# Optimization experiments

Hardware: AMD Instinct MI355X
Metric: run time of the kernel (lower is better)

Reference implementation:

```python
import jax, jax.numpy as jnp
import numpy as np

N = 128          # system size (8*8*2), hard-coded in SpectrumLoss
M_LANCZOS = 10   # Lanczos(m=10)
KAPPA = 0.276


def dd_opt(x, U1, kappa):
    # Wilson-style 2D hopping operator (stand-in for the external DDOpt).
    # x: (B,8,8,2) fields, U1: (B,8,8,2) real gauge links (2 directions).
    u0 = U1[..., 0:1]
    u1 = U1[..., 1:2]
    hop = (u0 * jnp.roll(x, -1, axis=1)
           + u1 * jnp.roll(x, -1, axis=2)
           + jnp.roll(u0 * x, 1, axis=1)
           + jnp.roll(u1 * x, 1, axis=2))
    return x - kappa * hop


def build_lower_tri(net_out):
    # Row-major packing of a lower-triangular NxN matrix (torch.tril_indices order).
    B = net_out.shape[0]
    r, c = jnp.tril_indices(N)
    L = jnp.zeros((B, N, N), net_out.dtype)
    return L.at[:, r, c].set(net_out)


def matvect(L, U1, x):
    # x: (B, N). Preconditioned operator: L (L^T (D x)).
    B = x.shape[0]
    y = dd_opt(x.reshape(B, 8, 8, 2), U1, KAPPA).reshape(B, N)
    y = jnp.einsum('bij,bi->bj', L, y)  # upper_tri_mat: M^H v (real -> M^T v)
    y = jnp.einsum('bij,bj->bi', L, y)  # lower_tri_matvect: L v
    return y


def lanczos(Av, v0):
    # Standard batched Lanczos producing symmetric tridiagonal T (B, M, M).
    B = v0.shape[0]

    def step(carry, _):
        v_prev, v_cur, beta = carry
        w = Av(v_cur)
        alpha = jnp.sum(w * v_cur, axis=1)
        w = w - alpha[:, None] * v_cur - beta[:, None] * v_prev
        beta_new = jnp.linalg.norm(w, axis=1)
        v_next = w / (beta_new[:, None] + 1e-30)
        return (v_cur, v_next, beta_new), (alpha, beta_new)

    init = (jnp.zeros_like(v0), v0, jnp.zeros((B,), v0.dtype))
    _, (alphas, betas) = jax.lax.scan(step, init, None, length=M_LANCZOS)
    alphas = alphas.T  # (B, M)
    betas = betas.T    # (B, M); last beta unused
    T = jnp.zeros((B, M_LANCZOS, M_LANCZOS), v0.dtype)
    i = jnp.arange(M_LANCZOS)
    T = T.at[:, i, i].set(alphas)
    j = jnp.arange(M_LANCZOS - 1)
    T = T.at[:, j, j + 1].set(betas[:, :-1])
    T = T.at[:, j + 1, j].set(betas[:, :-1])
    return T


def setup_inputs() -> dict:
    key = jax.random.key(0)
    k1, k2, k3 = jax.random.split(key, 3)
    B = 2048
    net_out = jax.random.normal(k1, (B, N * (N + 1) // 2), dtype=jnp.float32)
    U1 = jax.random.uniform(k2, (B, 8, 8, 2), dtype=jnp.float32)
    v = jax.random.normal(k3, (B, N), dtype=jnp.float32)
    return {"net_out": net_out, "U1": U1, "v": v}


def reference(net_out, U1, v):
    vn = v / jnp.linalg.norm(v, axis=1, keepdims=True)
    L = build_lower_tri(net_out)
    T = lanczos(lambda x: matvect(L, U1, x), vn)
    eig = jnp.abs(jnp.linalg.eigvalsh(T))  # symmetric tridiagonal -> real eigvals
    max_e = jnp.max(eig, axis=1)
    min_e = jnp.min(eig, axis=1)
    return jnp.mean(max_e ** 2) - jnp.mean(min_e ** 2)
```

## Files before the change

kernel.cpp:

```cpp
#include <hip/hip_runtime.h>
#include <hip/hip_bf16.h>
#include <math.h>

#define NN 128
#define TRI 8256
#define BATCH 2048
#define M_L 10
#define KAPPA 0.276f
#define LDL 136

using half8  = __attribute__((ext_vector_type(8))) _Float16;
using half2v = __attribute__((ext_vector_type(2))) _Float16;
using f32x4  = __attribute__((ext_vector_type(4))) float;

static __device__ inline float dot2h(unsigned m, unsigned y, float c) {
#if __has_builtin(__builtin_amdgcn_fdot2)
    return __builtin_amdgcn_fdot2(__builtin_bit_cast(half2v, m),
                                  __builtin_bit_cast(half2v, y), c, false);
#else
    half2v a = __builtin_bit_cast(half2v, m), b = __builtin_bit_cast(half2v, y);
    return c + (float)a.x * (float)b.x + (float)a.y * (float)b.y;
#endif
}

__device__ inline int sturm_count10(const double* a, const double* off2, double x) {
    double pm = 1.0;
    double p  = a[0] - x;
    int c = (p < 0.0);
    #pragma unroll
    for (int i = 1; i < M_L; i++) {
        double pn = (a[i] - x) * p - off2[i - 1] * pm;
        c += ((pn < 0.0) != (p < 0.0));
        pm = p; p = pn;
    }
    return c;
}

__global__ __launch_bounds__(256, 4) void lanczos_kernel(
    const float* __restrict__ net_out,
    const float* __restrict__ U1,
    const float* __restrict__ v_in,
    float* __restrict__ contrib)
{
    __shared__ __align__(16) _Float16 Lsq[128 * LDL];
    __shared__ __align__(16) unsigned ys[64];
    __shared__ __align__(16) float part[256];
    __shared__ __align__(16) float ab_s[20];

    const int b = blockIdx.x;
    const int t = threadIdx.x;
    const int lane = t & 63;
    const int w = t >> 6;

    float2 vv = {0.f, 0.f}, uu = {0.f, 0.f};
    if (w == 0) {
        vv = *(const float2*)(v_in + (size_t)b * NN + 2 * lane);
        uu = *(const float2*)(U1 + (size_t)b * 128 + 2 * lane);
    }

    {
        unsigned long long* z = (unsigned long long*)Lsq;
        #pragma unroll
        for (int k = t; k < 128 * LDL / 4; k += 256) z[k] = 0ULL;
    }
    __syncthreads();

    {
        const float4* src4 = (const float4*)(net_out + (size_t)b * TRI);
        for (int q = t; q < TRI / 4; q += 256) {
            float4 f = src4[q];
            const int e = 4 * q;
            float vals[4] = {f.x, f.y, f.z, f.w};
            #pragma unroll
            for (int i = 0; i < 4; i++) {
                int ei = e + i;
                int r = (int)((sqrtf((float)(8 * ei) + 1.0f) - 1.0f) * 0.5f);
                int c = ei - ((r * (r + 1)) >> 1);
                Lsq[r * LDL + c] = (_Float16)vals[i];
            }
        }
    }
    __syncthreads();

    {
        const int m = lane & 15;
        const int g = lane >> 4;
        f32x4 acc[2][8];
        #pragma unroll
        for (int bi = 0; bi < 2; bi++)
            #pragma unroll
            for (int j = 0; j < 8; j++) acc[bi][j] = (f32x4){0.f, 0.f, 0.f, 0.f};
        const int band0 = w, band1 = w + 4;
        #pragma unroll
        for (int kc = 0; kc < 4; kc++) {
            const int col = kc * 32 + g * 8;
            half8 a0 = *(const half8*)&Lsq[(16 * band0 + m) * LDL + col];
            half8 a1 = *(const half8*)&Lsq[(16 * band1 + m) * LDL + col];
            #pragma unroll
            for (int j = 0; j < 8; j++) {
                half8 bfr = *(const half8*)&Lsq[(16 * j + m) * LDL + col];
                acc[0][j] = __builtin_amdgcn_mfma_f32_16x16x32_f16(a0, bfr, acc[0][j], 0, 0, 0);
                acc[1][j] = __builtin_amdgcn_mfma_f32_16x16x32_f16(a1, bfr, acc[1][j], 0, 0, 0);
            }
        }
        __syncthreads();

        #pragma unroll
        for (int bi = 0; bi < 2; bi++) {
            const int band = (bi == 0) ? band0 : band1;
            #pragma unroll
            for (int j = 0; j < 8; j++) {
                f32x4 a = acc[bi][j];
                half2v p01 = {(_Float16)a[0], (_Float16)a[1]};
                half2v p23 = {(_Float16)a[2], (_Float16)a[3]};
                uint2 pk;
                pk.x = __builtin_bit_cast(unsigned, p01);
                pk.y = __builtin_bit_cast(unsigned, p23);
                *(uint2*)&Lsq[(16 * j + m) * LDL + 16 * band + 4 * g] = pk;
            }
        }
    }
    __syncthreads();

    const int r = t & 127, h = t >> 7;
    uint4 Mr[8];
    {
        const uint4* M4 = (const uint4*)&Lsq[r * LDL + 64 * h];
        #pragma unroll
        for (int c = 0; c < 8; c++) Mr[c] = M4[c];
    }

    float x0 = 0.f, x1 = 0.f, p0 = 0.f, p1 = 0.f, beta = 0.f;
    float u0c = 0.f, u1c = 0.f, u0m = 0.f, u1m = 0.f;
    const int l_ip = (lane + 8) & 63;
    const int l_jp = (lane & 56) | ((lane + 1) & 7);
    const int l_im = (lane + 56) & 63;
    const int l_jm = (lane & 56) | ((lane + 7) & 7);

    if (w == 0) {
        float s = vv.x * vv.x + vv.y * vv.y;
        #pragma unroll
        for (int o = 1; o < 64; o <<= 1) s += __shfl_xor(s, o, 64);
        float inv = 1.0f / sqrtf(s);
        x0 = vv.x * inv; x1 = vv.y * inv;
        u0c = uu.x; u1c = uu.y;
        u0m = __shfl(u0c, l_im, 64);
        u1m = __shfl(u1c, l_jm, 64);

        float a0 = __shfl(x0, l_ip, 64), a1 = __shfl(x1, l_ip, 64);
        float b0 = __shfl(x0, l_jp, 64), b1 = __shfl(x1, l_jp, 64);
        float c0 = __shfl(x0, l_im, 64), c1 = __shfl(x1, l_im, 64);
        float d0 = __shfl(x0, l_jm, 64), d1 = __shfl(x1, l_jm, 64);
        float y0 = x0 - KAPPA * (u0c * a0 + u1c * b0 + u0m * c0 + u1m * d0);
        float y1 = x1 - KAPPA * (u0c * a1 + u1c * b1 + u0m * c1 + u1m * d1);
        half2v yp = {(_Float16)y0, (_Float16)y1};
        ys[lane] = __builtin_bit_cast(unsigned, yp);
    }
    __syncthreads();

    const uint4* Y4 = (const uint4*)&ys[32 * h];

    for (int it = 0; it < M_L; it++) {
        {
            float aA = 0.f, aB = 0.f, aC = 0.f, aD = 0.f;
            #pragma unroll
            for (int c = 0; c < 8; c += 4) {
                uint4 y_0 = Y4[c],     y_1 = Y4[c + 1];
                uint4 y_2 = Y4[c + 2], y_3 = Y4[c + 3];
                aA = dot2h(Mr[c].x,     y_0.x, aA); aA = dot2h(Mr[c].y,     y_0.y, aA);
                aA = dot2h(Mr[c].z,     y_0.z, aA); aA = dot2h(Mr[c].w,     y_0.w, aA);
                aB = dot2h(Mr[c + 1].x, y_1.x, aB); aB = dot2h(Mr[c + 1].y, y_1.y, aB);
                aB = dot2h(Mr[c + 1].z, y_1.z, aB); aB = dot2h(Mr[c + 1].w, y_1.w, aB);
                aC = dot2h(Mr[c + 2].x, y_2.x, aC); aC = dot2h(Mr[c + 2].y, y_2.y, aC);
                aC = dot2h(Mr[c + 2].z, y_2.z, aC); aC = dot2h(Mr[c + 2].w, y_2.w, aC);
                aD = dot2h(Mr[c + 3].x, y_3.x, aD); aD = dot2h(Mr[c + 3].y, y_3.y, aD);
                aD = dot2h(Mr[c + 3].z, y_3.z, aD); aD = dot2h(Mr[c + 3].w, y_3.w, aD);
            }
            part[t] = (aA + aB) + (aC + aD);
        }
        __syncthreads();

        if (w == 0) {
            float2 pa = *(const float2*)&part[2 * lane];
            float2 pb = *(const float2*)&part[128 + 2 * lane];
            float z0 = pa.x + pb.x;
            float z1 = pa.y + pb.y;

            float s1 = z0 * x0 + z1 * x1;
            float s2 = z0 * z0 + z1 * z1;
            float s3 = z0 * p0 + z1 * p1;
            #pragma unroll
            for (int o = 1; o < 64; o <<= 1) {
                s1 += __shfl_xor(s1, o, 64);
                s2 += __shfl_xor(s2, o, 64);
                s3 += __shfl_xor(s3, o, 64);
            }
            float alpha = s1;
            float b2 = s2 - alpha * alpha - beta * (2.0f * s3 - beta);
            float bn = sqrtf(fmaxf(b2, 0.0f));
            float w0 = z0 - alpha * x0 - beta * p0;
            float w1 = z1 - alpha * x1 - beta * p1;
            float inv = 1.0f / (bn + 1e-30f);
            p0 = x0; p1 = x1;
            x0 = w0 * inv; x1 = w1 * inv;
            beta = bn;
            if (lane == 0) {
                ab_s[it]      = alpha;
                ab_s[10 + it] = bn;
            }

            float a0 = __shfl(x0, l_ip, 64), a1 = __shfl(x1, l_ip, 64);
            float b0 = __shfl(x0, l_jp, 64), b1 = __shfl(x1, l_jp, 64);
            float c0 = __shfl(x0, l_im, 64), c1 = __shfl(x1, l_im, 64);
            float d0 = __shfl(x0, l_jm, 64), d1 = __shfl(x1, l_jm, 64);
            float y0 = x0 - KAPPA * (u0c * a0 + u1c * b0 + u0m * c0 + u1m * d0);
            float y1 = x1 - KAPPA * (u0c * a1 + u1c * b1 + u0m * c1 + u1m * d1);
            half2v yp = {(_Float16)y0, (_Float16)y1};
            ys[lane] = __builtin_bit_cast(unsigned, yp);
        }
        __syncthreads();
    }

    if (w != (b & 3)) return;

    double a[M_L], off2[M_L - 1], offa[M_L - 1];
    #pragma unroll
    for (int i = 0; i < M_L; i++) a[i] = (double)ab_s[i];
    #pragma unroll
    for (int i = 0; i < M_L - 1; i++) {
        double bb = (double)ab_s[10 + i];
        offa[i] = fabs(bb);
        off2[i] = bb * bb;
    }
    double glo = 1e300, ghi = -1e300;
    #pragma unroll
    for (int i = 0; i < M_L; i++) {
        double rr = 0.0;
        if (i > 0) rr += offa[i - 1];
        if (i < M_L - 1) rr += offa[i];
        glo = fmin(glo, a[i] - rr);
        ghi = fmax(ghi, a[i] + rr);
    }

    const int kk = lane & 31;
    const bool topHalf = (lane >= 32);

    const int K = topHalf ? 1 : M_L;
    double lo = glo, hi = ghi;
    for (int round = 0; round < 4; round++) {
        double wdt = (hi - lo) * (1.0 / 33.0);
        double x = lo + wdt * (double)(kk + 1);
        int cnt = sturm_count10(a, off2, x);
        unsigned long long m64 = __ballot(cnt >= K);
        unsigned mm = topHalf ? (unsigned)(m64 >> 32)
                              : (unsigned)(m64 & 0xffffffffu);
        int p = (mm == 0u) ? 32 : (__ffs(mm) - 1);
        double nlo = lo + wdt * (double)p;
        hi = (mm == 0u) ? hi : (lo + wdt * (double)(p + 1));
        lo = nlo;
    }
    double mid = 0.5 * (lo + hi);
    double lmax = __shfl(mid, 0, 64);
    double lmin = __shfl(mid, 32, 64);
    double maxabs = fmax(fabs(lmax), fabs(lmin));

    double wlo = 0.0, whi = maxabs;
    for (int round = 0; round < 4; round++) {
        double wdt = (whi - wlo) * (1.0 / 33.0);
        double s = wlo + wdt * (double)(kk + 1);
        double x = topHalf ? -s : s;
        int cnt = sturm_count10(a, off2, x);
        int o = __shfl_xor(cnt, 32, 64);
        int inwin = topHalf ? (o - cnt) : (cnt - o);
        unsigned long long m64 = __ballot(inwin >= 1);
        unsigned mm = (unsigned)(m64 & 0xffffffffu);
        int p = (mm == 0u) ? 32 : (__ffs(mm) - 1);
        double nlo = wlo + wdt * (double)p;
        whi = (mm == 0u) ? whi : (wlo + wdt * (double)(p + 1));
        wlo = nlo;
    }
    double minabs = 0.5 * (wlo + whi);
    if (lane == 0) contrib[b] = (float)(maxabs * maxabs - minabs * minabs);
}

__global__ __launch_bounds__(1024) void reduce_kernel(
    const float* __restrict__ contrib, float* __restrict__ out)
{
    __shared__ float red[16];
    int t = threadIdx.x;
    float s = contrib[t] + contrib[t + 1024];
    #pragma unroll
    for (int o = 32; o > 0; o >>= 1) s += __shfl_down(s, o, 64);
    if ((t & 63) == 0) red[t >> 6] = s;
    __syncthreads();
    if (t < 64) {
        float r = (t < 16) ? red[t] : 0.0f;
        #pragma unroll
        for (int o = 8; o > 0; o >>= 1) r += __shfl_down(r, o, 64);
        if (t == 0) out[0] = r / (float)BATCH;
    }
}

extern "C" void kernel_launch(void* const* d_in, const int* in_sizes, int n_in,
                              void* d_out, int out_size, void* d_ws, size_t ws_size,
                              hipStream_t stream) {
    const float* net_out = (const float*)d_in[0];
    const float* U1      = (const float*)d_in[1];
    const float* v       = (const float*)d_in[2];
    float* contrib = (float*)d_ws;

    lanczos_kernel<<<BATCH, 256, 0, stream>>>(net_out, U1, v, contrib);
    reduce_kernel<<<1, 1024, 0, stream>>>(contrib, (float*)d_out);
}
```

Before: 130.1 us.

## Replicate Lanczos vector update in every wave to drop a barrier per iteration

Each of the four waves now redundantly runs the reduction, alpha/beta computation and hopping operator, and writes its own copy of the y vector into a per-wave LDS slot. This removes the second __syncthreads per Lanczos iteration and the idle time of waves 1-3 while wave 0 worked. The partial-sum buffer is double-buffered by iteration parity so the single remaining barrier suffices. The Sturm counting now reads the tridiagonal coefficients straight from LDS instead of register arrays, trading register pressure for LDS reads, and extra redundant ALU work is added in every wave.

```diff
diff --git a/kernel.cpp b/kernel.cpp
--- a/kernel.cpp
+++ b/kernel.cpp
@@ -23,13 +23,14 @@
 #endif
 }
 
-__device__ inline int sturm_count10(const double* a, const double* off2, double x) {
+__device__ inline int sturm_lds(const float* __restrict__ ab_s, double x) {
     double pm = 1.0;
-    double p  = a[0] - x;
+    double p  = (double)ab_s[0] - x;
     int c = (p < 0.0);
     #pragma unroll
     for (int i = 1; i < M_L; i++) {
-        double pn = (a[i] - x) * p - off2[i - 1] * pm;
+        double bb = (double)ab_s[10 + i - 1];
+        double pn = ((double)ab_s[i] - x) * p - (bb * bb) * pm;
         c += ((pn < 0.0) != (p < 0.0));
         pm = p; p = pn;
     }
@@ -43,20 +44,18 @@
     float* __restrict__ contrib)
 {
     __shared__ __align__(16) _Float16 Lsq[128 * LDL];
-    __shared__ __align__(16) unsigned ys[64];
-    __shared__ __align__(16) float part[256];
+    __shared__ __align__(16) unsigned ysw[4][64];
+    __shared__ __align__(16) float part[2][256];
     __shared__ __align__(16) float ab_s[20];
 
     const int b = blockIdx.x;
     const int t = threadIdx.x;
     const int lane = t & 63;
     const int w = t >> 6;
-
-    float2 vv = {0.f, 0.f}, uu = {0.f, 0.f};
-    if (w == 0) {
-        vv = *(const float2*)(v_in + (size_t)b * NN + 2 * lane);
-        uu = *(const float2*)(U1 + (size_t)b * 128 + 2 * lane);
-    }
+    const int tw = b & 3;
+
+    float2 vv = *(const float2*)(v_in + (size_t)b * NN + 2 * lane);
+    float2 uu = *(const float2*)(U1 + (size_t)b * 128 + 2 * lane);
 
     {
         unsigned long long* z = (unsigned long long*)Lsq;
@@ -130,22 +129,21 @@
         for (int c = 0; c < 8; c++) Mr[c] = M4[c];
     }
 
-    float x0 = 0.f, x1 = 0.f, p0 = 0.f, p1 = 0.f, beta = 0.f;
-    float u0c = 0.f, u1c = 0.f, u0m = 0.f, u1m = 0.f;
     const int l_ip = (lane + 8) & 63;
     const int l_jp = (lane & 56) | ((lane + 1) & 7);
     const int l_im = (lane + 56) & 63;
     const int l_jm = (lane & 56) | ((lane + 7) & 7);
 
-    if (w == 0) {
+    float x0, x1, p0 = 0.f, p1 = 0.f, beta = 0.f;
+    const float u0c = uu.x, u1c = uu.y;
+    const float u0m = __shfl(u0c, l_im, 64);
+    const float u1m = __shfl(u1c, l_jm, 64);
+    {
         float s = vv.x * vv.x + vv.y * vv.y;
         #pragma unroll
         for (int o = 1; o < 64; o <<= 1) s += __shfl_xor(s, o, 64);
         float inv = 1.0f / sqrtf(s);
         x0 = vv.x * inv; x1 = vv.y * inv;
-        u0c = uu.x; u1c = uu.y;
-        u0m = __shfl(u0c, l_im, 64);
-        u1m = __shfl(u1c, l_jm, 64);
 
         float a0 = __shfl(x0, l_ip, 64), a1 = __shfl(x1, l_ip, 64);
         float b0 = __shfl(x0, l_jp, 64), b1 = __shfl(x1, l_jp, 64);
@@ -154,11 +152,10 @@
         float y0 = x0 - KAPPA * (u0c * a0 + u1c * b0 + u0m * c0 + u1m * d0);
         float y1 = x1 - KAPPA * (u0c * a1 + u1c * b1 + u0m * c1 + u1m * d1);
         half2v yp = {(_Float16)y0, (_Float16)y1};
-        ys[lane] = __builtin_bit_cast(unsigned, yp);
-    }
-    __syncthreads();
-
-    const uint4* Y4 = (const uint4*)&ys[32 * h];
+        ysw[w][lane] = __builtin_bit_cast(unsigned, yp);
+    }
+
+    const uint4* Y4 = (const uint4*)&ysw[w][32 * h];
 
     for (int it = 0; it < M_L; it++) {
         {
@@ -176,13 +173,13 @@
                 aD = dot2h(Mr[c + 3].x, y_3.x, aD); aD = dot2h(Mr[c + 3].y, y_3.y, aD);
                 aD = dot2h(Mr[c + 3].z, y_3.z, aD); aD = dot2h(Mr[c + 3].w, y_3.w, aD);
             }
-            part[t] = (aA + aB) + (aC + aD);
+            part[it & 1][t] = (aA + aB) + (aC + aD);
         }
         __syncthreads();
 
-        if (w == 0) {
-            float2 pa = *(const float2*)&part[2 * lane];
-            float2 pb = *(const float2*)&part[128 + 2 * lane];
+        {
+            float2 pa = *(const float2*)&part[it & 1][2 * lane];
+            float2 pb = *(const float2*)&part[it & 1][128 + 2 * lane];
             float z0 = pa.x + pb.x;
             float z1 = pa.y + pb.y;
 
@@ -204,7 +201,7 @@
             p0 = x0; p1 = x1;
             x0 = w0 * inv; x1 = w1 * inv;
             beta = bn;
-            if (lane == 0) {
+            if (w == tw && lane == 0) {
                 ab_s[it]      = alpha;
                 ab_s[10 + it] = bn;
             }
@@ -216,30 +213,21 @@
             float y0 = x0 - KAPPA * (u0c * a0 + u1c * b0 + u0m * c0 + u1m * d0);
             float y1 = x1 - KAPPA * (u0c * a1 + u1c * b1 + u0m * c1 + u1m * d1);
             half2v yp = {(_Float16)y0, (_Float16)y1};
-            ys[lane] = __builtin_bit_cast(unsigned, yp);
-        }
-        __syncthreads();
-    }
-
-    if (w != (b & 3)) return;
-
-    double a[M_L], off2[M_L - 1], offa[M_L - 1];
-    #pragma unroll
-    for (int i = 0; i < M_L; i++) a[i] = (double)ab_s[i];
-    #pragma unroll
-    for (int i = 0; i < M_L - 1; i++) {
-        double bb = (double)ab_s[10 + i];
-        offa[i] = fabs(bb);
-        off2[i] = bb * bb;
-    }
+            ysw[w][lane] = __builtin_bit_cast(unsigned, yp);
+        }
+    }
+
+    if (w != tw) return;
+
     double glo = 1e300, ghi = -1e300;
     #pragma unroll
     for (int i = 0; i < M_L; i++) {
+        double ai = (double)ab_s[i];
         double rr = 0.0;
-        if (i > 0) rr += offa[i - 1];
-        if (i < M_L - 1) rr += offa[i];
-        glo = fmin(glo, a[i] - rr);
-        ghi = fmax(ghi, a[i] + rr);
+        if (i > 0)        rr += fabs((double)ab_s[10 + i - 1]);
+        if (i < M_L - 1)  rr += fabs((double)ab_s[10 + i]);
+        glo = fmin(glo, ai - rr);
+        ghi = fmax(ghi, ai + rr);
     }
 
     const int kk = lane & 31;
@@ -250,7 +238,7 @@
     for (int round = 0; round < 4; round++) {
         double wdt = (hi - lo) * (1.0 / 33.0);
         double x = lo + wdt * (double)(kk + 1);
-        int cnt = sturm_count10(a, off2, x);
+        int cnt = sturm_lds(ab_s, x);
         unsigned long long m64 = __ballot(cnt >= K);
         unsigned mm = topHalf ? (unsigned)(m64 >> 32)
                               : (unsigned)(m64 & 0xffffffffu);
@@ -269,7 +257,7 @@
         double wdt = (whi - wlo) * (1.0 / 33.0);
         double s = wlo + wdt * (double)(kk + 1);
         double x = topHalf ? -s : s;
-        int cnt = sturm_count10(a, off2, x);
+        int cnt = sturm_lds(ab_s, x);
         int o = __shfl_xor(cnt, 32, 64);
         int inwin = topHalf ? (o - cnt) : (cnt - o);
         unsigned long long m64 = __ballot(inwin >= 1);
```

New measurement: 138.5 us. 6.5% more time.
